# Performance work log

Hardware: AMD Instinct MI355X
Metric: run time of the kernel (lower is better)

## Reference

```python
import math
import jax, jax.numpy as jnp
import numpy as np
from jax.scipy.linalg import solve_triangular

K, D, Q = 512, 2048, 8
B = 8192
EPS = 1e-5
RHO0 = math.log(math.exp(1.0) - 1.0)  # softplus^-1(1.0), matches psi_init=scale_init=1.0


def setup_inputs() -> dict:
    key = jax.random.key(0)
    k1, k2, k3, k4, k5 = jax.random.split(key, 5)
    x = jax.random.normal(k1, (B, D), dtype=jnp.float32)
    mu = jax.random.normal(k2, (K, D), dtype=jnp.float32)          # centroids
    dir_raw = jax.random.normal(k3, (K, D, Q), dtype=jnp.float32) / math.sqrt(D)
    scale_rho = jnp.full((K, Q), RHO0, dtype=jnp.float32) + 0.01 * jax.random.normal(k4, (K, Q), dtype=jnp.float32)
    psi_rho = jnp.full((D,), RHO0, dtype=jnp.float32) + 0.01 * jax.random.normal(k5, (D,), dtype=jnp.float32)
    pi_logits = jnp.zeros((K,), dtype=jnp.float32)
    return {"x": x, "mu": mu, "dir_raw": dir_raw, "scale_rho": scale_rho,
            "psi_rho": psi_rho, "pi_logits": pi_logits}


def _nll(x, mu, dir_raw, scale_rho, psi_rho, pi_logits):
    Dd = x.shape[1]
    q = dir_raw.shape[2]
    # diagonal noise (shared across components since psi_per_component=False)
    psi = jax.nn.softplus(psi_rho) + EPS                      # (D,)
    psi_inv = 1.0 / psi                                       # (D,)
    # factor loadings W_k = normalize(dir_raw, dim=1) * softplus(scale)
    n = jnp.maximum(jnp.linalg.norm(dir_raw, axis=1, keepdims=True), EPS)
    W = (dir_raw / n) * jax.nn.softplus(scale_rho)[:, None, :]  # (K, D, q)
    # Woodbury inner matrix M_k = I + W^T Psi^{-1} W and its Cholesky
    A = W * jnp.sqrt(psi_inv)[None, :, None]                  # (K, D, q)
    M = jnp.einsum('kdi,kdj->kij', A, A) + jnp.eye(q, dtype=W.dtype)[None]
    L = jnp.linalg.cholesky(M)                                # (K, q, q) lower
    # quadratic form pieces
    xT_Pinv_x = (x ** 2) @ psi_inv                            # (B,)
    xT_Pinv_mu = x @ (psi_inv[None, :] * mu).T                # (B, K)
    muT_Pinv_mu = jnp.sum(mu ** 2 * psi_inv[None, :], axis=-1)  # (K,)
    quad_Psi = xT_Pinv_x[:, None] - 2.0 * xT_Pinv_mu + muT_Pinv_mu[None, :]
    PinvW = psi_inv[None, :, None] * W                        # (K, D, q)
    WT_Pinv_x = jnp.einsum('bd,kdq->bkq', x, PinvW)           # (B, K, q)
    WT_Pinv_mu = jnp.einsum('kd,kdq->kq', mu, PinvW)          # (K, q)
    v = WT_Pinv_x - WT_Pinv_mu[None, :, :]                    # (B, K, q)
    # Ez = M^{-1} v via the Cholesky factor (batched over K, rhs over B)
    vT = jnp.transpose(v, (1, 2, 0))                          # (K, q, B)
    y = solve_triangular(L, vT, lower=True)
    EzT = solve_triangular(jnp.swapaxes(L, -1, -2), y, lower=False)
    Ez = jnp.transpose(EzT, (2, 0, 1))                        # (B, K, q)
    quad = quad_Psi - jnp.sum(v * Ez, axis=-1)                # (B, K)
    # log-determinants via Woodbury: log|C| = log|Psi| + log|M|
    logdet_Psi = jnp.sum(jnp.log(psi))                        # scalar (shared psi)
    logdet_M = 2.0 * jnp.sum(jnp.log(jnp.diagonal(L, axis1=-2, axis2=-1)), axis=-1)  # (K,)
    logdet_C = logdet_Psi + logdet_M                          # (K,)
    ll = -0.5 * (Dd * math.log(2.0 * math.pi) + logdet_C[None, :] + quad)  # (B, K)
    log_pi = jax.nn.log_softmax(pi_logits)
    logp = jax.scipy.special.logsumexp(ll + log_pi[None, :], axis=1)  # (B,)
    return jnp.mean(-logp)


def reference(x, mu, dir_raw, scale_rho, psi_rho, pi_logits):
    return _nll(x, mu, dir_raw, scale_rho, psi_rho, pi_logits)
```

## Files before the change

kernel.cpp:

```cpp
#include <hip/hip_runtime.h>

constexpr int Bn = 8192;
constexpr int Dd = 2048;
constexpr int Kk = 512;
constexpr int Qq = 8;
constexpr int Nn = Kk * 9;
constexpr float DLOG2PI = 3763.9722f;

constexpr int BM = 128, BN = 144, BK = 128;

constexpr float SX = 16.f;
constexpr float SW = 64.f;
constexpr float SG = 16.f;
constexpr float INV_UW = 1.f / (16.f * 64.f);
constexpr float INV_UG = 1.f / (16.f * 16.f);

constexpr size_t OFF_PSI   = 0;
constexpr size_t OFF_LDP   = 8192;
constexpr size_t OFF_LOGPI = 8448;
constexpr size_t OFF_OFFK  = 10752;
constexpr size_t OFF_MINV  = 13056;
constexpr size_t OFF_XPX   = 144384;
constexpr size_t OFF_XBF   = 177408;
constexpr size_t OFF_GT    = 33731840;
constexpr size_t OFF_LL    = 52606208;
constexpr size_t OFF_PART  = 69383424;

typedef float f32x4 __attribute__((ext_vector_type(4)));
typedef int   i32x4v __attribute__((ext_vector_type(4)));
typedef int   i32x8v __attribute__((ext_vector_type(8)));

__device__ inline float softplusf(float x) {
  return fmaxf(x, 0.f) + log1pf(expf(-fabsf(x)));
}
__device__ inline unsigned char f2fp8(float x) {
  int v = __builtin_amdgcn_cvt_pk_fp8_f32(x, 0.f, 0, false);
  return (unsigned char)(v & 0xff);
}
__device__ inline void glds16(const unsigned char* g, char* l) {
  __builtin_amdgcn_global_load_lds(
      (const __attribute__((address_space(1))) unsigned int*)g,
      (__attribute__((address_space(3))) unsigned int*)l, 16, 0, 0);
}
__device__ inline i32x8v ld_frag(const char* rowp, int quad, int s8) {
  i32x4v lo = *(const i32x4v*)(rowp + (((2 * quad)     ^ s8) * 16));
  i32x4v hi = *(const i32x4v*)(rowp + (((2 * quad + 1) ^ s8) * 16));
  i32x8v r;
  r[0] = lo[0]; r[1] = lo[1]; r[2] = lo[2]; r[3] = lo[3];
  r[4] = hi[0]; r[5] = hi[1]; r[6] = hi[2]; r[7] = hi[3];
  return r;
}

__global__ __launch_bounds__(256) void prep_psi(
    const float* __restrict__ psi_rho, const float* __restrict__ pi_logits,
    float* __restrict__ psi_inv, float* __restrict__ logdetPsi,
    float* __restrict__ logpi) {
  __shared__ float red[256];
  int t = threadIdx.x;
  float acc = 0.f;
  for (int d = t; d < Dd; d += 256) {
    float p = softplusf(psi_rho[d]) + 1e-5f;
    psi_inv[d] = 1.f / p;
    acc += logf(p);
  }
  red[t] = acc;
  __syncthreads();
  for (int s = 128; s > 0; s >>= 1) { if (t < s) red[t] += red[t + s]; __syncthreads(); }
  if (t == 0) *logdetPsi = red[0];
  __syncthreads();
  float mx = -3.4e38f;
  for (int i = t; i < Kk; i += 256) mx = fmaxf(mx, pi_logits[i]);
  red[t] = mx;
  __syncthreads();
  for (int s = 128; s > 0; s >>= 1) { if (t < s) red[t] = fmaxf(red[t], red[t + s]); __syncthreads(); }
  mx = red[0];
  __syncthreads();
  float se = 0.f;
  for (int i = t; i < Kk; i += 256) se += expf(pi_logits[i] - mx);
  red[t] = se;
  __syncthreads();
  for (int s = 128; s > 0; s >>= 1) { if (t < s) red[t] += red[t + s]; __syncthreads(); }
  float lse = mx + logf(red[0]);
  for (int i = t; i < Kk; i += 256) logpi[i] = pi_logits[i] - lse;
}

__global__ __launch_bounds__(256) void prep_k(
    const float* __restrict__ mu, const float* __restrict__ dir_raw,
    const float* __restrict__ scale_rho, const float* __restrict__ psi_inv,
    const float* __restrict__ logdetPsi, const float* __restrict__ logpi,
    float* __restrict__ offk, float* __restrict__ Minv,
    unsigned char* __restrict__ Gq) {
  int k = blockIdx.x, t = threadIdx.x, lane = t & 63, w = t >> 6;
  float vals[53];
#pragma unroll
  for (int i = 0; i < 53; i++) vals[i] = 0.f;
  const float4* dirp = (const float4*)(dir_raw + (size_t)k * Dd * Qq);
  for (int d = t; d < Dd; d += 256) {
    float4 da = dirp[d * 2], db = dirp[d * 2 + 1];
    float dir8[8] = {da.x, da.y, da.z, da.w, db.x, db.y, db.z, db.w};
    float pw = psi_inv[d];
    float md = mu[(size_t)k * Dd + d];
    int c = 0;
#pragma unroll
    for (int i = 0; i < 8; i++) {
      float dip = dir8[i] * pw;
#pragma unroll
      for (int j = 0; j < 8; j++) {
        if (j < i) continue;
        vals[c] += dip * dir8[j]; c++;
      }
    }
#pragma unroll
    for (int q = 0; q < 8; q++) vals[36 + q] += dir8[q] * dir8[q];
    float mp = md * pw;
#pragma unroll
    for (int q = 0; q < 8; q++) vals[44 + q] += mp * dir8[q];
    vals[52] += md * mp;
  }
  __shared__ float redk[4 * 53];
#pragma unroll
  for (int v = 0; v < 53; v++) {
    float val = vals[v];
#pragma unroll
    for (int o = 32; o; o >>= 1) val += __shfl_down(val, o, 64);
    if (lane == 0) redk[w * 53 + v] = val;
  }
  __syncthreads();
  __shared__ float R[53];
  __shared__ float sAl[8], sHh[8];
  if (t < 53) R[t] = redk[t] + redk[53 + t] + redk[106 + t] + redk[159 + t];
  __syncthreads();
  if (t == 0) {
    float Sf[8][8];
    {
      int c2 = 0;
#pragma unroll
      for (int i = 0; i < 8; i++) {
#pragma unroll
        for (int j = 0; j < 8; j++) {
          if (j < i) continue;
          float v = R[c2++]; Sf[i][j] = v; Sf[j][i] = v;
        }
      }
    }
    float alpha[8];
#pragma unroll
    for (int q = 0; q < 8; q++) {
      float nr = fmaxf(sqrtf(R[36 + q]), 1e-5f);
      alpha[q] = softplusf(scale_rho[(size_t)k * 8 + q]) / nr;
    }
    float Mm[8][8];
#pragma unroll
    for (int i = 0; i < 8; i++)
#pragma unroll
      for (int j = 0; j < 8; j++)
        Mm[i][j] = alpha[i] * alpha[j] * Sf[i][j] + (i == j ? 1.f : 0.f);
    float L[8][8], Ld[8];
#pragma unroll
    for (int i = 0; i < 8; i++) {
#pragma unroll
      for (int j = 0; j < 8; j++) {
        if (j > i) continue;
        float s2 = Mm[i][j];
#pragma unroll
        for (int p = 0; p < 8; p++) { if (p < j) s2 -= L[i][p] * L[j][p]; }
        if (i == j) { L[i][i] = sqrtf(s2); Ld[i] = 1.f / L[i][i]; }
        else        L[i][j] = s2 * Ld[j];
      }
    }
    float logdetM = 0.f;
#pragma unroll
    for (int i = 0; i < 8; i++) logdetM += 2.f * logf(L[i][i]);
    float wv[8];
#pragma unroll
    for (int q = 0; q < 8; q++) wv[q] = alpha[q] * R[44 + q];
    float y[8], h[8];
#pragma unroll
    for (int i = 0; i < 8; i++) {
      float s2 = wv[i];
#pragma unroll
      for (int p = 0; p < 8; p++) { if (p < i) s2 -= L[i][p] * y[p]; }
      y[i] = s2 * Ld[i];
    }
#pragma unroll
    for (int i = 7; i >= 0; i--) {
      float s2 = y[i];
#pragma unroll
      for (int p = 0; p < 8; p++) { if (p > i) s2 -= L[p][i] * h[p]; }
      h[i] = s2 * Ld[i];
    }
    float cc = R[52];
#pragma unroll
    for (int q = 0; q < 8; q++) cc -= wv[q] * h[q];
#pragma unroll
    for (int col = 0; col < 8; col++) {
      float yy[8], z[8];
#pragma unroll
      for (int i = 0; i < 8; i++) {
        float s2 = (i == col) ? 1.f : 0.f;
#pragma unroll
        for (int p = 0; p < 8; p++) { if (p < i) s2 -= L[i][p] * yy[p]; }
        yy[i] = s2 * Ld[i];
      }
#pragma unroll
      for (int i = 7; i >= 0; i--) {
        float s2 = yy[i];
#pragma unroll
        for (int p = 0; p < 8; p++) { if (p > i) s2 -= L[p][i] * z[p]; }
        z[i] = s2 * Ld[i];
      }
#pragma unroll
      for (int r2 = 0; r2 < 8; r2++) Minv[(size_t)k * 64 + r2 * 8 + col] = z[r2];
    }
    offk[k] = -0.5f * (DLOG2PI + logdetPsi[0] + logdetM + cc) + logpi[k];
#pragma unroll
    for (int q = 0; q < 8; q++) { sAl[q] = alpha[q]; sHh[q] = h[q]; }
  }
  __syncthreads();
  float al[8], hh[8];
#pragma unroll
  for (int q = 0; q < 8; q++) { al[q] = sAl[q]; hh[q] = sHh[q]; }
  for (int d = t; d < Dd; d += 256) {
    float4 da = dirp[d * 2], db = dirp[d * 2 + 1];
    float dir8[8] = {da.x, da.y, da.z, da.w, db.x, db.y, db.z, db.w};
    float pw = psi_inv[d];
    float md = mu[(size_t)k * Dd + d];
    float gs = 0.f;
#pragma unroll
    for (int q = 0; q < 8; q++) {
      Gq[((size_t)(k * 9 + q)) * Dd + d] = f2fp8(SW * pw * al[q] * dir8[q]);
      gs += al[q] * dir8[q] * hh[q];
    }
    Gq[((size_t)(k * 9 + 8)) * Dd + d] = f2fp8(SG * pw * (md - gs));
  }
}

__global__ __launch_bounds__(256) void prep_x(
    const float* __restrict__ x, const float* __restrict__ psi_inv,
    unsigned char* __restrict__ xq, float* __restrict__ xPx) {
  int b = blockIdx.x, t = threadIdx.x, lane = t & 63, w = t >> 6;
  const float4* xr = (const float4*)(x + (size_t)b * Dd);
  const float4* pr = (const float4*)psi_inv;
  float4 v0 = xr[2 * t], v1 = xr[2 * t + 1];
  float4 p0 = pr[2 * t], p1 = pr[2 * t + 1];
  float acc = v0.x * v0.x * p0.x + v0.y * v0.y * p0.y + v0.z * v0.z * p0.z + v0.w * v0.w * p0.w
            + v1.x * v1.x * p1.x + v1.y * v1.y * p1.y + v1.z * v1.z * p1.z + v1.w * v1.w * p1.w;
  unsigned int q0 = (unsigned int)__builtin_amdgcn_cvt_pk_fp8_f32(SX * v0.x, SX * v0.y, 0, false);
  q0 = (unsigned int)__builtin_amdgcn_cvt_pk_fp8_f32(SX * v0.z, SX * v0.w, (int)q0, true);
  unsigned int q1 = (unsigned int)__builtin_amdgcn_cvt_pk_fp8_f32(SX * v1.x, SX * v1.y, 0, false);
  q1 = (unsigned int)__builtin_amdgcn_cvt_pk_fp8_f32(SX * v1.z, SX * v1.w, (int)q1, true);
  uint2 o; o.x = q0; o.y = q1;
  *(uint2*)(xq + (size_t)b * Dd + t * 8) = o;
#pragma unroll
  for (int s2 = 32; s2; s2 >>= 1) acc += __shfl_down(acc, s2, 64);
  __shared__ float r4[4];
  if (lane == 0) r4[w] = acc;
  __syncthreads();
  if (t == 0) xPx[b] = r4[0] + r4[1] + r4[2] + r4[3];
}

__global__ __launch_bounds__(256, 3) void gemm_ll(
    const unsigned char* __restrict__ xq, const unsigned char* __restrict__ Gq,
    const float* __restrict__ Minv, const float* __restrict__ offk,
    const float* __restrict__ xPx, float* __restrict__ ll) {
  __shared__ char smem[42112];
  float* Cs    = (float*)smem;
  float* sMinv = (float*)(smem + 37888);
  float* sOff  = (float*)(smem + 37888 + 4160);

  int t = threadIdx.x, lane = t & 63, w = t >> 6;
  int m0 = blockIdx.y * BM;
  int n0 = blockIdx.x * BN;
  int comp0 = blockIdx.x * 16;

  for (int i = t; i < 1024; i += 256) {
    int cl = i >> 6, idx = i & 63;
    sMinv[cl * 65 + idx] = Minv[(size_t)comp0 * 64 + i];
  }
  if (t < 16) sOff[t] = offk[comp0 + t];

  f32x4 acc[2][9];
  f32x4 zero = {0.f, 0.f, 0.f, 0.f};
#pragma unroll
  for (int mt = 0; mt < 2; mt++)
#pragma unroll
    for (int nt = 0; nt < 9; nt++) acc[mt][nt] = zero;

  int rr  = lane >> 3;
  int cph = lane & 7;
  int csw = cph ^ rr;
  int quad = lane >> 4, r16 = lane & 15;
  int s8 = r16 & 7;

  for (int k0 = 0; k0 < Dd; k0 += BK) {
    __syncthreads();
#pragma unroll
    for (int j = 0; j < 4; ++j) {
      int jj = w * 4 + j;
      glds16(xq + (size_t)(m0 + jj * 8 + rr) * Dd + k0 + csw * 16,
             smem + jj * 1024);
    }
    for (int jj = w; jj < 18; jj += 4) {
      glds16(Gq + (size_t)(n0 + jj * 8 + rr) * Dd + k0 + csw * 16,
             smem + 16384 + jj * 1024);
    }
    __syncthreads();
    i32x8v a0 = ld_frag(smem + (w * 32 + r16) * 128, quad, s8);
    i32x8v a1 = ld_frag(smem + (w * 32 + 16 + r16) * 128, quad, s8);
#pragma unroll
    for (int nt = 0; nt < 9; ++nt) {
      i32x8v bv = ld_frag(smem + 16384 + (nt * 16 + r16) * 128, quad, s8);
      acc[0][nt] = __builtin_amdgcn_mfma_scale_f32_16x16x128_f8f6f4(
          a0, bv, acc[0][nt], 0, 0, 0, 0x7f7f7f7f, 0, 0x7f7f7f7f);
      acc[1][nt] = __builtin_amdgcn_mfma_scale_f32_16x16x128_f8f6f4(
          a1, bv, acc[1][nt], 0, 0, 0, 0x7f7f7f7f, 0, 0x7f7f7f7f);
    }
  }

  float P[36];
  {
    const float* Mi = sMinv + r16 * 65;
    int c = 0;
#pragma unroll
    for (int i2 = 0; i2 < 8; i2++) {
      P[c++] = 0.5f * Mi[i2 * 8 + i2];
#pragma unroll
      for (int j2 = i2 + 1; j2 < 8; j2++) P[c++] = Mi[i2 * 8 + j2];
    }
  }
  float offc = sOff[r16];

  float* myC = Cs + w * (16 * 148);
#pragma unroll
  for (int mt = 0; mt < 2; ++mt) {
    __syncthreads();
#pragma unroll
    for (int nt = 0; nt < 9; ++nt) {
#pragma unroll
      for (int r = 0; r < 4; r++) {
        myC[(quad * 4 + r) * 148 + nt * 16 + r16] = acc[mt][nt][r];
      }
    }
    __syncthreads();
#pragma unroll
    for (int i = 0; i < 4; i++) {
      int row_l = quad + 4 * i;
      int b = m0 + w * 32 + mt * 16 + row_l;
      const float* cp = myC + row_l * 148 + r16 * 9;
      float u[8];
#pragma unroll
      for (int j = 0; j < 8; j++) u[j] = cp[j] * INV_UW;
      float s = cp[8] * INV_UG;
      float tq = 0.f;
      int c = 0;
#pragma unroll
      for (int i2 = 0; i2 < 8; i2++) {
        float s2 = P[c++] * u[i2];
#pragma unroll
        for (int j2 = i2 + 1; j2 < 8; j2++) s2 += P[c++] * u[j2];
        tq += u[i2] * s2;
      }
      ll[(size_t)b * Kk + comp0 + r16] = offc + s + tq - 0.5f * xPx[b];
    }
  }
}

__global__ __launch_bounds__(256) void lse_rows(
    const float* __restrict__ ll, float* __restrict__ part) {
  int t = threadIdx.x, lane = t & 63, w = t >> 6;
  int b = blockIdx.x * 4 + w;
  const float* row = ll + (size_t)b * Kk;
  float v[8];
  float mx = -3.4e38f;
#pragma unroll
  for (int i = 0; i < 8; i++) { v[i] = row[lane + 64 * i]; mx = fmaxf(mx, v[i]); }
#pragma unroll
  for (int o = 32; o; o >>= 1) mx = fmaxf(mx, __shfl_xor(mx, o, 64));
  float se = 0.f;
#pragma unroll
  for (int i = 0; i < 8; i++) se += expf(v[i] - mx);
#pragma unroll
  for (int o = 32; o; o >>= 1) se += __shfl_xor(se, o, 64);
  __shared__ float r4[4];
  if (lane == 0) r4[w] = -(mx + logf(se));
  __syncthreads();
  if (t == 0) part[blockIdx.x] = r4[0] + r4[1] + r4[2] + r4[3];
}

__global__ __launch_bounds__(256) void final_mean(
    const float* __restrict__ part, float* __restrict__ out) {
  int t = threadIdx.x, lane = t & 63, w = t >> 6;
  float acc = 0.f;
  for (int i = t; i < 2048; i += 256) acc += part[i];
#pragma unroll
  for (int o = 32; o; o >>= 1) acc += __shfl_down(acc, o, 64);
  __shared__ float r4[4];
  if (lane == 0) r4[w] = acc;
  __syncthreads();
  if (t == 0) out[0] = (r4[0] + r4[1] + r4[2] + r4[3]) * (1.0f / 8192.0f);
}

extern "C" void kernel_launch(void* const* d_in, const int* in_sizes, int n_in,
                              void* d_out, int out_size, void* d_ws, size_t ws_size,
                              hipStream_t stream) {
  const float* x         = (const float*)d_in[0];
  const float* mu        = (const float*)d_in[1];
  const float* dir_raw   = (const float*)d_in[2];
  const float* scale_rho = (const float*)d_in[3];
  const float* psi_rho   = (const float*)d_in[4];
  const float* pi_logits = (const float*)d_in[5];
  float* out = (float*)d_out;
  char* ws = (char*)d_ws;

  float* psi_inv          = (float*)(ws + OFF_PSI);
  float* logdetPsi        = (float*)(ws + OFF_LDP);
  float* logpi            = (float*)(ws + OFF_LOGPI);
  float* offk             = (float*)(ws + OFF_OFFK);
  float* Minv             = (float*)(ws + OFF_MINV);
  float* xPx              = (float*)(ws + OFF_XPX);
  unsigned char* xq       = (unsigned char*)(ws + OFF_XBF);
  unsigned char* Gq       = (unsigned char*)(ws + OFF_GT);
  float* ll               = (float*)(ws + OFF_LL);
  float* part             = (float*)(ws + OFF_PART);

  prep_psi<<<1, 256, 0, stream>>>(psi_rho, pi_logits, psi_inv, logdetPsi, logpi);
  prep_k<<<Kk, 256, 0, stream>>>(mu, dir_raw, scale_rho, psi_inv, logdetPsi, logpi,
                                 offk, Minv, Gq);
  prep_x<<<Bn, 256, 0, stream>>>(x, psi_inv, xq, xPx);
  dim3 g(Nn / BN, Bn / BM);
  gemm_ll<<<g, 256, 0, stream>>>(xq, Gq, Minv, offk, xPx, ll);
  lse_rows<<<Bn / 4, 256, 0, stream>>>(ll, part);
  final_mean<<<1, 256, 0, stream>>>(part, out);
}
```

Before: 255.4 us.

## Double GEMM M-tile to 256 rows and cache prescaled directions in prep LDS

```diff
diff --git a/kernel.cpp b/kernel.cpp
--- a/kernel.cpp
+++ b/kernel.cpp
@@ -7,7 +7,7 @@
 constexpr int Nn = Kk * 9;
 constexpr float DLOG2PI = 3763.9722f;
 
-constexpr int BM = 128, BN = 144, BK = 128;
+constexpr int BM = 256, BN = 144, BK = 128;
 
 constexpr float SX = 16.f;
 constexpr float SW = 64.f;
@@ -32,6 +32,15 @@
 
 __device__ inline float softplusf(float x) {
   return fmaxf(x, 0.f) + log1pf(expf(-fabsf(x)));
+}
+__device__ inline unsigned short f2bf(float x) {
+  unsigned int u = __builtin_bit_cast(unsigned int, x);
+  u = (u + 0x7fffu + ((u >> 16) & 1u)) >> 16;
+  return (unsigned short)u;
+}
+__device__ inline float bf2f(unsigned short u) {
+  unsigned int v = ((unsigned int)u) << 16;
+  return __builtin_bit_cast(float, v);
 }
 __device__ inline unsigned char f2fp8(float x) {
   int v = __builtin_amdgcn_cvt_pk_fp8_f32(x, 0.f, 0, false);
@@ -90,6 +99,8 @@
     const float* __restrict__ logdetPsi, const float* __restrict__ logpi,
     float* __restrict__ offk, float* __restrict__ Minv,
     unsigned char* __restrict__ Gq) {
+  __shared__ unsigned short sDir[Dd * 8];
+  __shared__ float sPwmd[Dd];
   int k = blockIdx.x, t = threadIdx.x, lane = t & 63, w = t >> 6;
   float vals[53];
 #pragma unroll
@@ -116,6 +127,9 @@
 #pragma unroll
     for (int q = 0; q < 8; q++) vals[44 + q] += mp * dir8[q];
     vals[52] += md * mp;
+#pragma unroll
+    for (int q = 0; q < 8; q++) sDir[d * 8 + q] = f2bf(pw * dir8[q]);
+    sPwmd[d] = mp;
   }
   __shared__ float redk[4 * 53];
 #pragma unroll
@@ -127,7 +141,7 @@
   }
   __syncthreads();
   __shared__ float R[53];
-  __shared__ float sAl[8], sHh[8];
+  __shared__ float sAl[8], sAh[8];
   if (t < 53) R[t] = redk[t] + redk[53 + t] + redk[106 + t] + redk[159 + t];
   __syncthreads();
   if (t == 0) {
@@ -214,24 +228,23 @@
     }
     offk[k] = -0.5f * (DLOG2PI + logdetPsi[0] + logdetM + cc) + logpi[k];
 #pragma unroll
-    for (int q = 0; q < 8; q++) { sAl[q] = alpha[q]; sHh[q] = h[q]; }
-  }
-  __syncthreads();
-  float al[8], hh[8];
-#pragma unroll
-  for (int q = 0; q < 8; q++) { al[q] = sAl[q]; hh[q] = sHh[q]; }
+    for (int q = 0; q < 8; q++) { sAl[q] = alpha[q]; sAh[q] = alpha[q] * h[q]; }
+  }
+  __syncthreads();
+  float al[8], ah[8];
+#pragma unroll
+  for (int q = 0; q < 8; q++) { al[q] = sAl[q]; ah[q] = sAh[q]; }
   for (int d = t; d < Dd; d += 256) {
-    float4 da = dirp[d * 2], db = dirp[d * 2 + 1];
-    float dir8[8] = {da.x, da.y, da.z, da.w, db.x, db.y, db.z, db.w};
-    float pw = psi_inv[d];
-    float md = mu[(size_t)k * Dd + d];
+    float pd[8];
+#pragma unroll
+    for (int q = 0; q < 8; q++) pd[q] = bf2f(sDir[d * 8 + q]);
     float gs = 0.f;
 #pragma unroll
     for (int q = 0; q < 8; q++) {
-      Gq[((size_t)(k * 9 + q)) * Dd + d] = f2fp8(SW * pw * al[q] * dir8[q]);
-      gs += al[q] * dir8[q] * hh[q];
-    }
-    Gq[((size_t)(k * 9 + 8)) * Dd + d] = f2fp8(SG * pw * (md - gs));
+      Gq[((size_t)(k * 9 + q)) * Dd + d] = f2fp8(SW * al[q] * pd[q]);
+      gs += ah[q] * pd[q];
+    }
+    Gq[((size_t)(k * 9 + 8)) * Dd + d] = f2fp8(SG * (sPwmd[d] - gs));
   }
 }
 
@@ -259,14 +272,14 @@
   if (t == 0) xPx[b] = r4[0] + r4[1] + r4[2] + r4[3];
 }
 
-__global__ __launch_bounds__(256, 3) void gemm_ll(
+__global__ __launch_bounds__(256, 2) void gemm_ll(
     const unsigned char* __restrict__ xq, const unsigned char* __restrict__ Gq,
     const float* __restrict__ Minv, const float* __restrict__ offk,
     const float* __restrict__ xPx, float* __restrict__ ll) {
-  __shared__ char smem[42112];
+  __shared__ char smem[55424];
   float* Cs    = (float*)smem;
-  float* sMinv = (float*)(smem + 37888);
-  float* sOff  = (float*)(smem + 37888 + 4160);
+  float* sMinv = (float*)(smem + 51200);
+  float* sOff  = (float*)(smem + 51200 + 4160);
 
   int t = threadIdx.x, lane = t & 63, w = t >> 6;
   int m0 = blockIdx.y * BM;
@@ -279,10 +292,10 @@
   }
   if (t < 16) sOff[t] = offk[comp0 + t];
 
-  f32x4 acc[2][9];
+  f32x4 acc[4][9];
   f32x4 zero = {0.f, 0.f, 0.f, 0.f};
 #pragma unroll
-  for (int mt = 0; mt < 2; mt++)
+  for (int mt = 0; mt < 4; mt++)
 #pragma unroll
     for (int nt = 0; nt < 9; nt++) acc[mt][nt] = zero;
 
@@ -292,28 +305,35 @@
   int quad = lane >> 4, r16 = lane & 15;
   int s8 = r16 & 7;
 
+#pragma unroll 1
   for (int k0 = 0; k0 < Dd; k0 += BK) {
     __syncthreads();
 #pragma unroll
-    for (int j = 0; j < 4; ++j) {
-      int jj = w * 4 + j;
+    for (int j = 0; j < 8; ++j) {
+      int jj = w * 8 + j;
       glds16(xq + (size_t)(m0 + jj * 8 + rr) * Dd + k0 + csw * 16,
              smem + jj * 1024);
     }
     for (int jj = w; jj < 18; jj += 4) {
       glds16(Gq + (size_t)(n0 + jj * 8 + rr) * Dd + k0 + csw * 16,
-             smem + 16384 + jj * 1024);
+             smem + 32768 + jj * 1024);
     }
     __syncthreads();
-    i32x8v a0 = ld_frag(smem + (w * 32 + r16) * 128, quad, s8);
-    i32x8v a1 = ld_frag(smem + (w * 32 + 16 + r16) * 128, quad, s8);
+    i32x8v a0 = ld_frag(smem + (w * 64 +      r16) * 128, quad, s8);
+    i32x8v a1 = ld_frag(smem + (w * 64 + 16 + r16) * 128, quad, s8);
+    i32x8v a2 = ld_frag(smem + (w * 64 + 32 + r16) * 128, quad, s8);
+    i32x8v a3 = ld_frag(smem + (w * 64 + 48 + r16) * 128, quad, s8);
 #pragma unroll
     for (int nt = 0; nt < 9; ++nt) {
-      i32x8v bv = ld_frag(smem + 16384 + (nt * 16 + r16) * 128, quad, s8);
+      i32x8v bv = ld_frag(smem + 32768 + (nt * 16 + r16) * 128, quad, s8);
       acc[0][nt] = __builtin_amdgcn_mfma_scale_f32_16x16x128_f8f6f4(
           a0, bv, acc[0][nt], 0, 0, 0, 0x7f7f7f7f, 0, 0x7f7f7f7f);
       acc[1][nt] = __builtin_amdgcn_mfma_scale_f32_16x16x128_f8f6f4(
           a1, bv, acc[1][nt], 0, 0, 0, 0x7f7f7f7f, 0, 0x7f7f7f7f);
+      acc[2][nt] = __builtin_amdgcn_mfma_scale_f32_16x16x128_f8f6f4(
+          a2, bv, acc[2][nt], 0, 0, 0, 0x7f7f7f7f, 0, 0x7f7f7f7f);
+      acc[3][nt] = __builtin_amdgcn_mfma_scale_f32_16x16x128_f8f6f4(
+          a3, bv, acc[3][nt], 0, 0, 0, 0x7f7f7f7f, 0, 0x7f7f7f7f);
     }
   }
 
@@ -330,10 +350,10 @@
   }
   float offc = sOff[r16];
 
+  __syncthreads();
   float* myC = Cs + w * (16 * 148);
 #pragma unroll
-  for (int mt = 0; mt < 2; ++mt) {
-    __syncthreads();
+  for (int mt = 0; mt < 4; ++mt) {
 #pragma unroll
     for (int nt = 0; nt < 9; ++nt) {
 #pragma unroll
@@ -341,11 +361,10 @@
         myC[(quad * 4 + r) * 148 + nt * 16 + r16] = acc[mt][nt][r];
       }
     }
-    __syncthreads();
 #pragma unroll
     for (int i = 0; i < 4; i++) {
       int row_l = quad + 4 * i;
-      int b = m0 + w * 32 + mt * 16 + row_l;
+      int b = m0 + w * 64 + mt * 16 + row_l;
       const float* cp = myC + row_l * 148 + r16 * 9;
       float u[8];
 #pragma unroll
```

Result: faster. 241.0 us (-5.6%).
